# Kernel optimization log

Measured on AMD Instinct MI355X. Metric: run time of the kernel, lower is better.

The kernel has to match this reference:

```python
import jax, jax.numpy as jnp
import numpy as np

LN_EPS = 1e-5


def _offdiag_idx(n):
    # flat row-major indices of the off-diagonal entries of an n x n matrix,
    # matching torch.masked_select order on ~eye(n)
    m = ~np.eye(n, dtype=bool)
    return jnp.asarray(np.flatnonzero(m.ravel()), dtype=jnp.int32)


def setup_inputs() -> dict:
    key = jax.random.key(0)
    ks = jax.random.split(key, 3)
    B, IN, OUT = 8192, 128, 128
    K = IN * (IN - 1)
    x = jax.random.normal(ks[0], (B, IN), dtype=jnp.float32)
    scale = jnp.ones((1, 1, IN), dtype=jnp.float32)
    translation = jnp.zeros((1, 1, IN), dtype=jnp.float32)
    # kaiming-uniform-like init
    bound_lc = np.sqrt(1.0 / K)
    lc_w = jax.random.uniform(ks[1], (OUT, K), minval=-bound_lc, maxval=bound_lc, dtype=jnp.float32)
    bound_w1 = np.sqrt(1.0 / IN)
    w1 = jax.random.uniform(ks[2], (OUT, IN), minval=-bound_w1, maxval=bound_w1, dtype=jnp.float32)
    gamma = jnp.ones((OUT,), dtype=jnp.float32)
    beta = jnp.zeros((OUT,), dtype=jnp.float32)
    return {"x": x, "scale": scale, "translation": translation,
            "lc_w": lc_w, "w1": w1, "gamma": gamma, "beta": beta}


def reference(x, scale, translation, lc_w, w1, gamma, beta):
    B, IN = x.shape
    idx = _offdiag_idx(IN)  # static [IN*(IN-1)]
    x_scaled = (x - translation[:, 0, :]) / scale[:, 0, :]          # [B, IN]
    pairwise = x_scaled[:, :, None] * x_scaled[:, None, :]          # [B, IN, IN]
    pairwise = pairwise.reshape(B, IN * IN)[:, idx]                 # [B, IN*(IN-1)]
    lc_out = pairwise @ lc_w.T                                      # [B, OUT]
    base = x @ w1.T                                                 # [B, OUT]
    y = lc_out + base
    mu = jnp.mean(y, axis=-1, keepdims=True)
    var = jnp.mean(jnp.square(y - mu), axis=-1, keepdims=True)
    return (y - mu) * jax.lax.rsqrt(var + LN_EPS) * gamma + beta
```

## Files before the change

### kernel.cpp

```cpp
#include <hip/hip_runtime.h>
#include <hip/hip_bf16.h>

typedef _Float16 f16;
typedef __attribute__((ext_vector_type(8))) _Float16 f16x8;
typedef __attribute__((ext_vector_type(4))) float f32x4;

#define IN 128
#define OUT 128
#define NB 8192
#define KSPLIT 4
#define CPK 32

#define WB_OFF   0ull
#define XH_OFF   4227072ull
#define BIAS_OFF 6324224ull
#define PARTS_OFF 6324736ull

__global__ __launch_bounds__(256) void prep_kernel(
    const float* __restrict__ x, const float* __restrict__ lcw, const float* __restrict__ w1,
    const float* __restrict__ sc, const float* __restrict__ tr,
    f16* __restrict__ WB, f16* __restrict__ xh, float* __restrict__ bias)
{
    const int bid = blockIdx.x;
    if (bid < 1032) {
        size_t idx = (size_t)bid * 2048 + (size_t)threadIdx.x * 8;
        int c   = (int)(idx >> 14);
        int rem = (int)(idx & 16383);
        int o   = rem >> 7;
        int j0  = rem & 127;
        f16x8 v;
        if (c < 128) {
            const float* lr = lcw + (size_t)o * 16256 + (size_t)c * 127;
            #pragma unroll
            for (int e = 0; e < 8; ++e) {
                int j = j0 + e;
                float f = (j == c) ? 0.f : lr[(j < c) ? j : (j - 1)];
                v[e] = (f16)f;
            }
        } else {
            #pragma unroll
            for (int e = 0; e < 8; ++e) {
                int j = j0 + e;
                v[e] = (f16)(w1[o * 128 + j] * sc[j]);
            }
        }
        *(f16x8*)(WB + idx) = v;
    } else if (bid < 1544) {
        size_t idx = (size_t)(bid - 1032) * 2048 + (size_t)threadIdx.x * 8;
        int j0 = (int)(idx & 127);
        const float4 x0 = *(const float4*)(x + idx);
        const float4 x1 = *(const float4*)(x + idx + 4);
        const float4 s0 = *(const float4*)(sc + j0);
        const float4 s1 = *(const float4*)(sc + j0 + 4);
        const float4 t0 = *(const float4*)(tr + j0);
        const float4 t1 = *(const float4*)(tr + j0 + 4);
        f16x8 v;
        v[0] = (f16)((x0.x - t0.x) / s0.x); v[1] = (f16)((x0.y - t0.y) / s0.y);
        v[2] = (f16)((x0.z - t0.z) / s0.z); v[3] = (f16)((x0.w - t0.w) / s0.w);
        v[4] = (f16)((x1.x - t1.x) / s1.x); v[5] = (f16)((x1.y - t1.y) / s1.y);
        v[6] = (f16)((x1.z - t1.z) / s1.z); v[7] = (f16)((x1.w - t1.w) / s1.w);
        *(f16x8*)(xh + idx) = v;
    } else {
        const int lane = threadIdx.x & 63;
        const int wv   = threadIdx.x >> 6;
        const float2 t2 = *(const float2*)(tr + lane * 2);
        for (int o = wv; o < 128; o += 4) {
            const float2 w2 = *(const float2*)(w1 + o * 128 + lane * 2);
            float s = t2.x * w2.x + t2.y * w2.y;
            #pragma unroll
            for (int m = 1; m < 64; m <<= 1) s += __shfl_xor(s, m);
            if (lane == 0) bias[o] = s;
        }
    }
}

__global__ __launch_bounds__(512, 1) void lc_gemm(
    const f16* __restrict__ xh, const f16* __restrict__ WB, float* __restrict__ parts)
{
    __shared__ f16 Bb[3][16384];
    __shared__ f16 xls[(CPK + 1) * 128];

    const int tid = threadIdx.x;
    const int bid = blockIdx.x;
    const int mt  = bid >> 2;
    const int kq  = bid & 3;
    const int row0 = mt << 7;

    const int lane = tid & 63;
    const int wv   = tid >> 6;
    const int wm   = wv >> 2;
    const int wn   = wv & 3;
    const int cl   = lane & 15;
    const int kg   = lane >> 4;

    const int c_lo = (kq == 0) ? 0 : (1 + kq * CPK);
    const int nc   = (kq == 0) ? (CPK + 1) : CPK;

    f16x8 ab[4][4];
    #pragma unroll
    for (int rb = 0; rb < 4; ++rb) {
        const size_t rw = (size_t)(row0 + wm * 64 + rb * 16 + cl) * IN;
        #pragma unroll
        for (int s = 0; s < 4; ++s)
            ab[rb][s] = *(const f16x8*)(xh + rw + s * 32 + kg * 8);
    }
    #pragma unroll
    for (int rb = 0; rb < 4; ++rb)
        #pragma unroll
        for (int s = 0; s < 4; ++s)
            asm volatile("" : "+v"(ab[rb][s]));

    int dmac[4];
    #pragma unroll
    for (int p = 0; p < 4; ++p) {
        int L = ((p * 8 + wv) << 10) | (lane << 4);
        dmac[p] = L ^ (((L >> 8) & 15) << 4);
    }
    int boff[2][4];
    #pragma unroll
    for (int cb = 0; cb < 2; ++cb)
        #pragma unroll
        for (int s = 0; s < 4; ++s) {
            int o = wn * 32 + cb * 16 + cl;
            boff[cb][s] = (o << 8) + ((((s << 2) + kg) ^ (o & 15)) << 4);
        }

    auto stageB = [&](int c, int buf) {
        const char* src = (const char*)WB + ((size_t)c << 15);
        #pragma unroll
        for (int p = 0; p < 4; ++p) {
            __builtin_amdgcn_global_load_lds(
                (const __attribute__((address_space(1))) unsigned int*)(src + dmac[p]),
                (__attribute__((address_space(3))) unsigned int*)((char*)(&Bb[buf][0]) + ((p * 8 + wv) << 10)),
                16, 0, 0);
        }
    };

    f32x4 acc[4][2];
    #pragma unroll
    for (int rb = 0; rb < 4; ++rb)
        #pragma unroll
        for (int cb = 0; cb < 2; ++cb)
            acc[rb][cb] = (f32x4){0.f, 0.f, 0.f, 0.f};

    for (int cp = tid >> 7; cp < nc; cp += 4) {
        int c = c_lo + cp;
        xls[cp * 128 + (tid & 127)] =
            (c < 128) ? xh[(size_t)(row0 + (tid & 127)) * IN + c] : (f16)1.0f;
    }
    stageB(c_lo + 0, 0);
    stageB(c_lo + 1, 1);
    __syncthreads();

#define KLOOP(NCV)                                                              \
    {                                                                           \
        constexpr int NC = NCV;                                                 \
        _Pragma("unroll")                                                       \
        for (int t = 0; t < NC; ++t) {                                          \
            if (t >= 1) {                                                       \
                if (t + 1 < NC) asm volatile("s_waitcnt vmcnt(4)" ::: "memory");\
                else            asm volatile("s_waitcnt vmcnt(0)" ::: "memory");\
                __builtin_amdgcn_s_barrier();                                   \
                __builtin_amdgcn_sched_barrier(0);                              \
            }                                                                   \
            if (t + 2 < NC) stageB(c_lo + t + 2, (t + 2) % 3);                  \
            const char* bbase = (const char*)(&Bb[t % 3][0]);                   \
            f16x8 bf[2][4];                                                     \
            _Pragma("unroll")                                                   \
            for (int cb = 0; cb < 2; ++cb)                                      \
                _Pragma("unroll")                                               \
                for (int s = 0; s < 4; ++s)                                     \
                    bf[cb][s] = *(const f16x8*)(bbase + boff[cb][s]);           \
            f16 xs[4];                                                          \
            _Pragma("unroll")                                                   \
            for (int rb = 0; rb < 4; ++rb)                                      \
                xs[rb] = xls[t * 128 + wm * 64 + rb * 16 + cl];                 \
            __builtin_amdgcn_s_setprio(1);                                      \
            _Pragma("unroll")                                                   \
            for (int s = 0; s < 4; ++s)                                         \
                _Pragma("unroll")                                               \
                for (int rb = 0; rb < 4; ++rb) {                                \
                    f16x8 xbv;                                                  \
                    _Pragma("unroll")                                           \
                    for (int e = 0; e < 8; ++e) xbv[e] = xs[rb];                \
                    f16x8 af = ab[rb][s] * xbv;                                 \
                    _Pragma("unroll")                                           \
                    for (int cb = 0; cb < 2; ++cb)                              \
                        acc[rb][cb] = __builtin_amdgcn_mfma_f32_16x16x32_f16(   \
                            af, bf[cb][s], acc[rb][cb], 0, 0, 0);               \
                }                                                               \
            __builtin_amdgcn_s_setprio(0);                                      \
        }                                                                       \
    }

    if (kq == 0) KLOOP(CPK + 1) else KLOOP(CPK)
#undef KLOOP

    float* po = parts + (size_t)kq * ((size_t)NB * OUT);
    #pragma unroll
    for (int rb = 0; rb < 4; ++rb) {
        const int grow = row0 + wm * 64 + rb * 16 + kg * 4;
        #pragma unroll
        for (int cb = 0; cb < 2; ++cb) {
            const int col = wn * 32 + cb * 16 + cl;
            #pragma unroll
            for (int q = 0; q < 4; ++q)
                po[(size_t)(grow + q) * OUT + col] = acc[rb][cb][q];
        }
    }
}

__global__ __launch_bounds__(256) void reduce_ln(
    const float* __restrict__ parts, const float* __restrict__ bias,
    const float* __restrict__ gamma, const float* __restrict__ beta,
    float* __restrict__ out)
{
    const int lane = threadIdx.x & 63;
    const int l5   = lane & 31;
    const int row  = blockIdx.x * 8 + (threadIdx.x >> 6) * 2 + (lane >> 5);
    const int c0   = l5 * 4;
    const size_t off = (size_t)row * OUT + c0;
    const size_t Q = (size_t)NB * OUT;

    float4 bb = *(const float4*)(bias + c0);
    float4 y = bb;
    #pragma unroll
    for (int k = 0; k < KSPLIT; ++k) {
        float4 p = *(const float4*)(parts + (size_t)k * Q + off);
        y.x += p.x; y.y += p.y; y.z += p.z; y.w += p.w;
    }

    float s  = y.x + y.y + y.z + y.w;
    float ss = y.x * y.x + y.y * y.y + y.z * y.z + y.w * y.w;
    #pragma unroll
    for (int m = 1; m < 32; m <<= 1) {
        s  += __shfl_xor(s, m);
        ss += __shfl_xor(ss, m);
    }
    const float mu  = s * (1.f / 128.f);
    const float var = ss * (1.f / 128.f) - mu * mu;
    const float rs  = rsqrtf(var + 1e-5f);

    float4 gg = *(const float4*)(gamma + c0);
    float4 be = *(const float4*)(beta + c0);
    float4 o4 = { (y.x - mu) * rs * gg.x + be.x, (y.y - mu) * rs * gg.y + be.y,
                  (y.z - mu) * rs * gg.z + be.z, (y.w - mu) * rs * gg.w + be.w };
    *(float4*)(out + off) = o4;
}

extern "C" void kernel_launch(void* const* d_in, const int* in_sizes, int n_in,
                              void* d_out, int out_size, void* d_ws, size_t ws_size,
                              hipStream_t stream) {
    const float* x     = (const float*)d_in[0];
    const float* sc    = (const float*)d_in[1];
    const float* tr    = (const float*)d_in[2];
    const float* lcw   = (const float*)d_in[3];
    const float* w1    = (const float*)d_in[4];
    const float* gamma = (const float*)d_in[5];
    const float* beta  = (const float*)d_in[6];
    float* out = (float*)d_out;

    char* ws = (char*)d_ws;
    f16*   WB    = (f16*)(ws + WB_OFF);
    f16*   xh    = (f16*)(ws + XH_OFF);
    float* bias  = (float*)(ws + BIAS_OFF);
    float* parts = (float*)(ws + PARTS_OFF);

    prep_kernel<<<1545, 256, 0, stream>>>(x, lcw, w1, sc, tr, WB, xh, bias);
    lc_gemm<<<256, 512, 0, stream>>>(xh, WB, parts);
    reduce_ln<<<1024, 256, 0, stream>>>(parts, bias, gamma, beta, out);
}
```

Measured before the change: 132.0 us.

## Split each K-chunk into two half-phases interleaving async B loads with MFMA

Splits the per-chunk B-tile prefetch into two halves issued between two MFMA phases, each phase reading only its half of B from LDS. A sched barrier and an extra workgroup barrier are added mid-chunk. The x broadcast vectors are also built once per chunk and reused. The aim is to spread global-to-LDS traffic and LDS reads across compute so they interleave better with the MFMAs. The cost is an additional s_barrier per chunk and tighter scheduling constraints.

```diff
diff --git a/kernel.cpp b/kernel.cpp
--- a/kernel.cpp
+++ b/kernel.cpp
@@ -125,10 +125,10 @@
             boff[cb][s] = (o << 8) + ((((s << 2) + kg) ^ (o & 15)) << 4);
         }
 
-    auto stageB = [&](int c, int buf) {
+    auto stageHalf = [&](int c, int buf, int h) {
         const char* src = (const char*)WB + ((size_t)c << 15);
         #pragma unroll
-        for (int p = 0; p < 4; ++p) {
+        for (int p = h * 2; p < h * 2 + 2; ++p) {
             __builtin_amdgcn_global_load_lds(
                 (const __attribute__((address_space(1))) unsigned int*)(src + dmac[p]),
                 (__attribute__((address_space(3))) unsigned int*)((char*)(&Bb[buf][0]) + ((p * 8 + wv) << 10)),
@@ -148,8 +148,8 @@
         xls[cp * 128 + (tid & 127)] =
             (c < 128) ? xh[(size_t)(row0 + (tid & 127)) * IN + c] : (f16)1.0f;
     }
-    stageB(c_lo + 0, 0);
-    stageB(c_lo + 1, 1);
+    stageHalf(c_lo + 0, 0, 0); stageHalf(c_lo + 0, 0, 1);
+    stageHalf(c_lo + 1, 1, 0); stageHalf(c_lo + 1, 1, 1);
     __syncthreads();
 
 #define KLOOP(NCV)                                                              \
@@ -163,33 +163,59 @@
                 __builtin_amdgcn_s_barrier();                                   \
                 __builtin_amdgcn_sched_barrier(0);                              \
             }                                                                   \
-            if (t + 2 < NC) stageB(c_lo + t + 2, (t + 2) % 3);                  \
             const char* bbase = (const char*)(&Bb[t % 3][0]);                   \
-            f16x8 bf[2][4];                                                     \
+                                          \
+            f16x8 bf0[2][2];                                                    \
             _Pragma("unroll")                                                   \
             for (int cb = 0; cb < 2; ++cb)                                      \
                 _Pragma("unroll")                                               \
-                for (int s = 0; s < 4; ++s)                                     \
-                    bf[cb][s] = *(const f16x8*)(bbase + boff[cb][s]);           \
-            f16 xs[4];                                                          \
-            _Pragma("unroll")                                                   \
-            for (int rb = 0; rb < 4; ++rb)                                      \
-                xs[rb] = xls[t * 128 + wm * 64 + rb * 16 + cl];                 \
+                for (int s = 0; s < 2; ++s)                                     \
+                    bf0[cb][s] = *(const f16x8*)(bbase + boff[cb][s]);          \
+            f16x8 xsp[4];                                                       \
+            _Pragma("unroll")                                                   \
+            for (int rb = 0; rb < 4; ++rb) {                                    \
+                f16 xv = xls[t * 128 + wm * 64 + rb * 16 + cl];                 \
+                _Pragma("unroll")                                               \
+                for (int e = 0; e < 8; ++e) xsp[rb][e] = xv;                    \
+            }                                                                   \
+            if (t + 2 < NC) stageHalf(c_lo + t + 2, (t + 2) % 3, 0);            \
+            __builtin_amdgcn_sched_barrier(0);                                  \
             __builtin_amdgcn_s_setprio(1);                                      \
             _Pragma("unroll")                                                   \
-            for (int s = 0; s < 4; ++s)                                         \
+            for (int s = 0; s < 2; ++s)                                         \
                 _Pragma("unroll")                                               \
                 for (int rb = 0; rb < 4; ++rb) {                                \
-                    f16x8 xbv;                                                  \
-                    _Pragma("unroll")                                           \
-                    for (int e = 0; e < 8; ++e) xbv[e] = xs[rb];                \
-                    f16x8 af = ab[rb][s] * xbv;                                 \
+                    f16x8 af = ab[rb][s] * xsp[rb];                             \
                     _Pragma("unroll")                                           \
                     for (int cb = 0; cb < 2; ++cb)                              \
                         acc[rb][cb] = __builtin_amdgcn_mfma_f32_16x16x32_f16(   \
-                            af, bf[cb][s], acc[rb][cb], 0, 0, 0);               \
+                            af, bf0[cb][s], acc[rb][cb], 0, 0, 0);              \
                 }                                                               \
             __builtin_amdgcn_s_setprio(0);                                      \
+            __builtin_amdgcn_sched_barrier(0);                                  \
+            __builtin_amdgcn_s_barrier();                                       \
+                                         \
+            f16x8 bf1[2][2];                                                    \
+            _Pragma("unroll")                                                   \
+            for (int cb = 0; cb < 2; ++cb)                                      \
+                _Pragma("unroll")                                               \
+                for (int s = 0; s < 2; ++s)                                     \
+                    bf1[cb][s] = *(const f16x8*)(bbase + boff[cb][s + 2]);      \
+            if (t + 2 < NC) stageHalf(c_lo + t + 2, (t + 2) % 3, 1);            \
+            __builtin_amdgcn_sched_barrier(0);                                  \
+            __builtin_amdgcn_s_setprio(1);                                      \
+            _Pragma("unroll")                                                   \
+            for (int s = 0; s < 2; ++s)                                         \
+                _Pragma("unroll")                                               \
+                for (int rb = 0; rb < 4; ++rb) {                                \
+                    f16x8 af = ab[rb][s + 2] * xsp[rb];                         \
+                    _Pragma("unroll")                                           \
+                    for (int cb = 0; cb < 2; ++cb)                              \
+                        acc[rb][cb] = __builtin_amdgcn_mfma_f32_16x16x32_f16(   \
+                            af, bf1[cb][s], acc[rb][cb], 0, 0, 0);              \
+                }                                                               \
+            __builtin_amdgcn_s_setprio(0);                                      \
+            __builtin_amdgcn_sched_barrier(0);                                  \
         }                                                                       \
     }
 
```

Measured after the change: 129.9 us. Within noise of the previous version (-1.6%).
